# Kernel optimization log

Hardware: AMD Instinct MI355X
Metric: run time of the kernel (lower is better)

Reference implementation:

```python
import jax, jax.numpy as jnp
import numpy as np

N = 8192
D = 256
E = 262144


def setup_inputs() -> dict:
    key = jax.random.key(0)
    kx, ke = jax.random.split(key)
    x = jax.random.normal(kx, (N, D), dtype=jnp.float32)
    edge_index = jax.random.randint(ke, (2, E), 0, N, dtype=jnp.int64)
    return {"x": x, "edge_index": edge_index}


def reference(x, edge_index):
    n, d = x.shape
    xs = x / (d ** 0.25)
    # per-edge similarity: equivalent to einsum('md,nd->mn')[src, dst] without O(n^2 d)
    src, dst = edge_index[0], edge_index[1]
    vals = jnp.einsum('ed,ed->e', xs[src], xs[dst])
    neg = jnp.finfo(jnp.float32).min
    sim = jnp.full((n, n), neg, dtype=x.dtype)
    sim = sim.at[src, dst].set(vals)
    # logaritmic=False branch: plain double softmax, averaged
    scores0 = jax.nn.softmax(sim, axis=1)                # row softmax
    scores1 = jax.nn.softmax(sim, axis=0)                # col softmax (== softmax(sim.T, -1).T)
    scores = (scores0 + scores1) * 0.5
    return scores, sim
```

## Files before the change

### kernel.cpp

```cpp
#include <hip/hip_runtime.h>
#include <float.h>
#include <math.h>

constexpr int Nn = 8192;
constexpr unsigned BG = 0xFF7F0000u;

typedef unsigned u32x4 __attribute__((ext_vector_type(4)));

__device__ __forceinline__ float clamp01(float f) {
    return fminf(fmaxf(f, 0.0f), 1.0f);
}
__device__ __forceinline__ unsigned f2bf(float f) {
    unsigned u = __float_as_uint(f);
    return (u + 0x7FFFu + ((u >> 16) & 1u)) >> 16;
}
__device__ __forceinline__ float lo16(unsigned u) { return __uint_as_float(u << 16); }
__device__ __forceinline__ float hi16(unsigned u) { return __uint_as_float(u & 0xFFFF0000u); }

__device__ __forceinline__ void load_edge(const unsigned* ew, unsigned F, int E, int e,
                                          int& s, int& d) {
    s = (int)(ew[e << F] & (Nn - 1));
    d = (int)(ew[(E << F) + (e << F)] & (Nn - 1));
}

__device__ __forceinline__ float stat_ss(float sr) {
    return sr + (sr == 0.0f ? (float)Nn : 0.0f);
}
__device__ __forceinline__ float stat_bgp(float sr) {
    return (sr == 0.0f) ? (1.0f / (float)Nn) : 0.0f;
}

__global__ void k1_conv(const float* __restrict__ x, unsigned* __restrict__ xb16,
                        const unsigned* __restrict__ ew, unsigned* __restrict__ flag,
                        float* __restrict__ rowsum, float* __restrict__ colsum) {
    int tid = blockIdx.x * 256 + threadIdx.x;
    const float4* xs = (const float4*)x + 2 * (size_t)tid;
    float4 a = xs[0];
    float4 c = xs[1];
    u32x4 p;
    p.x = f2bf(a.x) | (f2bf(a.y) << 16);
    p.y = f2bf(a.z) | (f2bf(a.w) << 16);
    p.z = f2bf(c.x) | (f2bf(c.y) << 16);
    p.w = f2bf(c.z) | (f2bf(c.w) << 16);
    ((u32x4*)xb16)[tid] = p;
    if (tid < Nn) {
        rowsum[tid] = 0.0f;
        colsum[tid] = 0.0f;
    }
    if (blockIdx.x == 0) {
        __shared__ unsigned acc;
        if (threadIdx.x == 0) acc = 0u;
        __syncthreads();
        atomicOr(&acc, ew[2 * threadIdx.x + 1]);
        __syncthreads();
        if (threadIdx.x == 0) flag[0] = (acc == 0u) ? 1u : 0u;
    }
}

__global__ void k2_edges(const unsigned* __restrict__ xb16, const unsigned* __restrict__ ew,
                         const unsigned* __restrict__ flag, float* __restrict__ sim,
                         float* __restrict__ vals,
                         float* __restrict__ rowsum, float* __restrict__ colsum, int E) {
    int lane = threadIdx.x & 63;
    int wid = threadIdx.x >> 6;
    int g = lane >> 3;
    int t = lane & 7;
    int e = (blockIdx.x * 4 + wid) * 8 + g;
    if (e >= E) return;
    unsigned F = flag[0];
    int s, d;
    load_edge(ew, F, E, e, s, d);
    const u32x4* xa = (const u32x4*)xb16 + (((size_t)s) << 5);
    const u32x4* xb = (const u32x4*)xb16 + (((size_t)d) << 5);
    float v = 0.0f;
    #pragma unroll
    for (int i = 0; i < 4; ++i) {
        u32x4 a = xa[t + 8 * i];
        u32x4 b = xb[t + 8 * i];
        v += lo16(a.x) * lo16(b.x) + hi16(a.x) * hi16(b.x);
        v += lo16(a.y) * lo16(b.y) + hi16(a.y) * hi16(b.y);
        v += lo16(a.z) * lo16(b.z) + hi16(a.z) * hi16(b.z);
        v += lo16(a.w) * lo16(b.w) + hi16(a.w) * hi16(b.w);
    }
    #pragma unroll
    for (int off = 4; off; off >>= 1) v += __shfl_xor(v, off);
    v *= 0.0625f;
    if (t == 0) {
        vals[e] = v;
        sim[(size_t)s * Nn + d] = v;
        float ev = expf(v);
        atomicAdd(&rowsum[s], ev);
        atomicAdd(&colsum[d], ev);
    }
}

__global__ void k3_out(const unsigned* __restrict__ ew, const unsigned* __restrict__ flag,
                       const float* __restrict__ vals,
                       const float* __restrict__ rowsum, const float* __restrict__ colsum,
                       float* __restrict__ scores, int E, int EB) {
    int b = blockIdx.x;
    if (b < EB) {
        int e = b * 256 + threadIdx.x;
        if (e >= E) return;
        unsigned F = flag[0];
        int s, d;
        load_edge(ew, F, E, e, s, d);
        float hr = 0.5f / stat_ss(rowsum[s]);
        float hc = 0.5f / stat_ss(colsum[d]);
        float sc = clamp01(expf(vals[e]) * (hr + hc));
        scores[(size_t)s * Nn + d] = sc;
        return;
    }
    for (int r = (b - EB) * 256 + threadIdx.x; r < 2 * Nn; r += 128 * 256) {
        if (r < Nn) {
            float ri = stat_bgp(rowsum[r]);
            if (ri == 0.0f) continue;
            for (int j = 0; j < Nn; ++j)
                scores[(size_t)r * Nn + j] = clamp01(0.5f * (ri + stat_bgp(colsum[j])));
        } else {
            int j = r - Nn;
            float cj = stat_bgp(colsum[j]);
            if (cj == 0.0f) continue;
            for (int i = 0; i < Nn; ++i)
                scores[(size_t)i * Nn + j] = clamp01(0.5f * (stat_bgp(rowsum[i]) + cj));
        }
    }
}

extern "C" void kernel_launch(void* const* d_in, const int* in_sizes, int n_in,
                              void* d_out, int out_size, void* d_ws, size_t ws_size,
                              hipStream_t stream) {
    const float* x = (const float*)d_in[0];
    const unsigned* ew = (const unsigned*)d_in[1];
    const int E = in_sizes[1] / 2;

    float* scores = (float*)d_out;
    float* sim = scores + (size_t)Nn * (size_t)Nn;

    char* w = (char*)d_ws;
    unsigned* flag = (unsigned*)w;  w += 16;
    float* vals = (float*)w;        w += (size_t)E * 4;
    unsigned* xb16 = (unsigned*)w;  w += (size_t)Nn * 256 / 2 * 4;
    float* rowsum = (float*)w;      w += (size_t)Nn * 4;
    float* colsum = (float*)w;      w += (size_t)Nn * 4;

    const int EB = (E + 255) / 256;

    hipMemsetD32Async((hipDeviceptr_t)sim, (int)BG, (size_t)Nn * (size_t)Nn, stream);
    k1_conv<<<1024, 256, 0, stream>>>(x, xb16, ew, flag, rowsum, colsum);
    k2_edges<<<(E + 31) / 32, 256, 0, stream>>>(xb16, ew, flag, sim, vals,
                                                rowsum, colsum, E);
    k3_out<<<EB + 128, 256, 0, stream>>>(ew, flag, vals, rowsum, colsum, scores, E, EB);
}
```

Baseline: 557.5 us.

## Fuse conversion, edge dot products and scoring into one cooperative kernel

Replaces the three kernel launches with a single cooperative kernel that uses grid-wide syncs between the bf16 conversion, the edge similarity/atomic-sum phase, and the score-writing phase. Each thread keeps up to eight edges' indices and values in registers across the sync, so the second phase does not reload edge indices or per-edge values from memory. This targets launch overhead and redundant global traffic, at the cost of grid-sync latency and a fixed 1024-block grid that must be co-resident. The 64 MB memset of sim remains the dominant cost.

```diff
diff --git a/kernel.cpp b/kernel.cpp
--- a/kernel.cpp
+++ b/kernel.cpp
@@ -1,9 +1,15 @@
 #include <hip/hip_runtime.h>
+#include <hip/hip_cooperative_groups.h>
 #include <float.h>
 #include <math.h>
 
+namespace cg = cooperative_groups;
+
 constexpr int Nn = 8192;
 constexpr unsigned BG = 0xFF7F0000u;
+constexpr int GRID = 1024;
+constexpr int ESTRIDE = GRID * 32;
+constexpr int ITER = 8;
 
 typedef unsigned u32x4 __attribute__((ext_vector_type(4)));
 
@@ -30,46 +36,7 @@
     return (sr == 0.0f) ? (1.0f / (float)Nn) : 0.0f;
 }
 
-__global__ void k1_conv(const float* __restrict__ x, unsigned* __restrict__ xb16,
-                        const unsigned* __restrict__ ew, unsigned* __restrict__ flag,
-                        float* __restrict__ rowsum, float* __restrict__ colsum) {
-    int tid = blockIdx.x * 256 + threadIdx.x;
-    const float4* xs = (const float4*)x + 2 * (size_t)tid;
-    float4 a = xs[0];
-    float4 c = xs[1];
-    u32x4 p;
-    p.x = f2bf(a.x) | (f2bf(a.y) << 16);
-    p.y = f2bf(a.z) | (f2bf(a.w) << 16);
-    p.z = f2bf(c.x) | (f2bf(c.y) << 16);
-    p.w = f2bf(c.z) | (f2bf(c.w) << 16);
-    ((u32x4*)xb16)[tid] = p;
-    if (tid < Nn) {
-        rowsum[tid] = 0.0f;
-        colsum[tid] = 0.0f;
-    }
-    if (blockIdx.x == 0) {
-        __shared__ unsigned acc;
-        if (threadIdx.x == 0) acc = 0u;
-        __syncthreads();
-        atomicOr(&acc, ew[2 * threadIdx.x + 1]);
-        __syncthreads();
-        if (threadIdx.x == 0) flag[0] = (acc == 0u) ? 1u : 0u;
-    }
-}
-
-__global__ void k2_edges(const unsigned* __restrict__ xb16, const unsigned* __restrict__ ew,
-                         const unsigned* __restrict__ flag, float* __restrict__ sim,
-                         float* __restrict__ vals,
-                         float* __restrict__ rowsum, float* __restrict__ colsum, int E) {
-    int lane = threadIdx.x & 63;
-    int wid = threadIdx.x >> 6;
-    int g = lane >> 3;
-    int t = lane & 7;
-    int e = (blockIdx.x * 4 + wid) * 8 + g;
-    if (e >= E) return;
-    unsigned F = flag[0];
-    int s, d;
-    load_edge(ew, F, E, e, s, d);
+__device__ __forceinline__ float dot_rows(const unsigned* xb16, int s, int d, int t) {
     const u32x4* xa = (const u32x4*)xb16 + (((size_t)s) << 5);
     const u32x4* xb = (const u32x4*)xb16 + (((size_t)d) << 5);
     float v = 0.0f;
@@ -84,34 +51,97 @@
     }
     #pragma unroll
     for (int off = 4; off; off >>= 1) v += __shfl_xor(v, off);
-    v *= 0.0625f;
-    if (t == 0) {
-        vals[e] = v;
-        sim[(size_t)s * Nn + d] = v;
-        float ev = expf(v);
-        atomicAdd(&rowsum[s], ev);
-        atomicAdd(&colsum[d], ev);
-    }
+    return v * 0.0625f;
 }
 
-__global__ void k3_out(const unsigned* __restrict__ ew, const unsigned* __restrict__ flag,
-                       const float* __restrict__ vals,
-                       const float* __restrict__ rowsum, const float* __restrict__ colsum,
-                       float* __restrict__ scores, int E, int EB) {
-    int b = blockIdx.x;
-    if (b < EB) {
-        int e = b * 256 + threadIdx.x;
-        if (e >= E) return;
-        unsigned F = flag[0];
+__global__ __launch_bounds__(256, 4) void k_fused(
+        const float* __restrict__ x, unsigned* __restrict__ xb16,
+        const unsigned* __restrict__ ew, float* __restrict__ sim,
+        float* __restrict__ vals, float* __restrict__ rowsum,
+        float* __restrict__ colsum, float* __restrict__ scores, int E) {
+    const int t = threadIdx.x;
+    const int gtid = blockIdx.x * 256 + t;
+
+    {
+        const float4* xs = (const float4*)x + 2 * (size_t)gtid;
+        float4 a = xs[0];
+        float4 c = xs[1];
+        u32x4 p;
+        p.x = f2bf(a.x) | (f2bf(a.y) << 16);
+        p.y = f2bf(a.z) | (f2bf(a.w) << 16);
+        p.z = f2bf(c.x) | (f2bf(c.y) << 16);
+        p.w = f2bf(c.z) | (f2bf(c.w) << 16);
+        ((u32x4*)xb16)[gtid] = p;
+        if (gtid < Nn) {
+            rowsum[gtid] = 0.0f;
+            colsum[gtid] = 0.0f;
+        }
+    }
+    const unsigned F = __syncthreads_or((int)(ew[2 * t + 1] != 0u)) ? 0u : 1u;
+
+    cg::this_grid().sync();
+
+    const int lane = t & 63;
+    const int wid = t >> 6;
+    const int g = lane >> 3;
+    const int st = lane & 7;
+    const int base = (blockIdx.x * 4 + wid) * 8 + g;
+
+    int sA[ITER], dA[ITER];
+    float vA[ITER];
+    #pragma unroll
+    for (int it = 0; it < ITER; ++it) {
+        sA[it] = 0; dA[it] = 0; vA[it] = 0.0f;
+        int e = base + it * ESTRIDE;
+        if (e < E) {
+            int s, d;
+            load_edge(ew, F, E, e, s, d);
+            sA[it] = s; dA[it] = d;
+            float v = dot_rows(xb16, s, d, st);
+            vA[it] = v;
+            if (st == 0) {
+                sim[(size_t)s * Nn + d] = v;
+                float ev = expf(v);
+                atomicAdd(&rowsum[s], ev);
+                atomicAdd(&colsum[d], ev);
+            }
+        }
+    }
+    for (int e = ITER * ESTRIDE + base; e < E; e += ESTRIDE) {
         int s, d;
         load_edge(ew, F, E, e, s, d);
-        float hr = 0.5f / stat_ss(rowsum[s]);
-        float hc = 0.5f / stat_ss(colsum[d]);
-        float sc = clamp01(expf(vals[e]) * (hr + hc));
-        scores[(size_t)s * Nn + d] = sc;
-        return;
+        float v = dot_rows(xb16, s, d, st);
+        if (st == 0) {
+            vals[e] = v;
+            sim[(size_t)s * Nn + d] = v;
+            float ev = expf(v);
+            atomicAdd(&rowsum[s], ev);
+            atomicAdd(&colsum[d], ev);
+        }
     }
-    for (int r = (b - EB) * 256 + threadIdx.x; r < 2 * Nn; r += 128 * 256) {
+
+    cg::this_grid().sync();
+
+    if (st == 0) {
+        #pragma unroll
+        for (int it = 0; it < ITER; ++it) {
+            int e = base + it * ESTRIDE;
+            if (e < E) {
+                float hr = 0.5f / stat_ss(rowsum[sA[it]]);
+                float hc = 0.5f / stat_ss(colsum[dA[it]]);
+                scores[(size_t)sA[it] * Nn + dA[it]] = clamp01(expf(vA[it]) * (hr + hc));
+            }
+        }
+        for (int e = ITER * ESTRIDE + base; e < E; e += ESTRIDE) {
+            int s, d;
+            load_edge(ew, F, E, e, s, d);
+            float hr = 0.5f / stat_ss(rowsum[s]);
+            float hc = 0.5f / stat_ss(colsum[d]);
+            scores[(size_t)s * Nn + d] = clamp01(expf(vals[e]) * (hr + hc));
+        }
+    }
+
+    for (int r = gtid; r < 2 * Nn; r += GRID * 256) {
         if (r < Nn) {
             float ri = stat_bgp(rowsum[r]);
             if (ri == 0.0f) continue;
@@ -132,23 +162,21 @@
                               hipStream_t stream) {
     const float* x = (const float*)d_in[0];
     const unsigned* ew = (const unsigned*)d_in[1];
-    const int E = in_sizes[1] / 2;
+    int E = in_sizes[1] / 2;
 
     float* scores = (float*)d_out;
     float* sim = scores + (size_t)Nn * (size_t)Nn;
 
     char* w = (char*)d_ws;
-    unsigned* flag = (unsigned*)w;  w += 16;
     float* vals = (float*)w;        w += (size_t)E * 4;
     unsigned* xb16 = (unsigned*)w;  w += (size_t)Nn * 256 / 2 * 4;
     float* rowsum = (float*)w;      w += (size_t)Nn * 4;
     float* colsum = (float*)w;      w += (size_t)Nn * 4;
 
-    const int EB = (E + 255) / 256;
+    hipMemsetD32Async((hipDeviceptr_t)sim, (int)BG, (size_t)Nn * (size_t)Nn, stream);
 
-    hipMemsetD32Async((hipDeviceptr_t)sim, (int)BG, (size_t)Nn * (size_t)Nn, stream);
-    k1_conv<<<1024, 256, 0, stream>>>(x, xb16, ew, flag, rowsum, colsum);
-    k2_edges<<<(E + 31) / 32, 256, 0, stream>>>(xb16, ew, flag, sim, vals,
-                                                rowsum, colsum, E);
-    k3_out<<<EB + 128, 256, 0, stream>>>(ew, flag, vals, rowsum, colsum, scores, E, EB);
+    void* args[] = {(void*)&x, (void*)&xb16, (void*)&ew, (void*)&sim, (void*)&vals,
+                    (void*)&rowsum, (void*)&colsum, (void*)&scores, (void*)&E};
+    hipLaunchCooperativeKernel((const void*)k_fused, dim3(GRID), dim3(256),
+                               args, 0, stream);
 }
```

Measured after the change: 769.4 us. 38.0% more time.
